# Kernel tuning notes

Hardware: AMD Instinct MI355X
Metric: run time of the kernel (lower is better)

Reference implementation:

```python
import jax, jax.numpy as jnp
import numpy as np

B, H, W = 2, 64, 1024
C1, C2 = 64, 128
MLP = [128, 128]
KH, KW = 5, 5
NS = 3
DIST = 100.0
BN_EPS = 1e-5


def setup_inputs() -> dict:
    key = jax.random.key(0)
    ks = jax.random.split(key, 12)
    inp = {
        "xyz1_proj": jax.random.normal(ks[0], (B, H, W, 3), jnp.float32),
        "xyz2_proj": jax.random.normal(ks[1], (B, H, W, 3), jnp.float32),
        "feat1_proj": jax.random.normal(ks[2], (B, H, W, C1), jnp.float32),
        "feat2_proj": jax.random.normal(ks[3], (B, H, W, C2), jnp.float32),
    }
    cin = C1 + C2
    chans = [cin] + MLP
    for i in range(len(MLP)):
        inp[f"w{i}"] = jax.random.normal(ks[4 + 2 * i], (chans[i], chans[i + 1]), jnp.float32) * 0.05
        inp[f"b{i}"] = jnp.zeros((chans[i + 1],), jnp.float32)
        inp[f"g{i}"] = jnp.ones((chans[i + 1],), jnp.float32)
        inp[f"be{i}"] = jnp.zeros((chans[i + 1],), jnp.float32)
    return inp


def _grid_knn(xyz1, xyz2):
    """Structured-grid KNN (no_sort_knn): for each query pixel, scan a KHxKW
    window in row-major order and take the first NS in-bounds neighbors whose
    squared distance is below DIST^2. Returns flat neighbor indices (B,N,NS)
    and a validity mask (B,N,NS,1)."""
    b, h, w, _ = xyz1.shape
    n = h * w
    k = KH * KW
    x1 = xyz1.reshape(b, n, 3)
    x2 = xyz2.reshape(b, n, 3)
    oh = jnp.repeat(jnp.arange(KH) - KH // 2, KW)   # (K,)
    ow = jnp.tile(jnp.arange(KW) - KW // 2, KH)     # (K,)
    nh = jnp.arange(h)[:, None, None] + oh[None, None, :]   # (H,1,K)
    nw = jnp.arange(w)[None, :, None] + ow[None, None, :]   # (1,W,K)
    inb = ((nh >= 0) & (nh < h)) & ((nw >= 0) & (nw < w))    # (H,W,K)
    flat = jnp.clip(nh, 0, h - 1) * w + jnp.clip(nw, 0, w - 1)
    flat = jnp.broadcast_to(flat, (h, w, k)).reshape(n, k)
    inb = jnp.broadcast_to(inb, (h, w, k)).reshape(n, k)
    # window gather: (B,N,K,3)
    neigh = jnp.take(x2, flat.reshape(-1), axis=1).reshape(b, n, k, 3)
    sq = jnp.sum(jnp.square(neigh - x1[:, :, None, :]), -1)  # (B,N,K)
    valid = inb[None] & (sq < DIST * DIST)
    v = valid.astype(jnp.int32)
    rank = jnp.cumsum(v, -1) - v  # rank among valid, scan order
    sel, fnd = [], []
    for j in range(NS):
        hit = valid & (rank == j)
        sel.append(jnp.argmax(hit, -1))
        fnd.append(jnp.any(hit, -1))
    sel = jnp.stack(sel, -1)          # (B,N,NS) window slot
    found = jnp.stack(fnd, -1)        # (B,N,NS)
    flat_b = jnp.broadcast_to(flat[None], (b, n, k))
    sel_flat = jnp.take_along_axis(flat_b, sel, axis=-1)
    sel_flat = jnp.where(found, sel_flat, 0)  # zeros like the init buffers
    mask = found.astype(x1.dtype)[..., None]  # (B,N,NS,1)
    return sel_flat, mask


def _gather(feat_flat, sel_flat):
    # feat_flat: (B,N,C), sel_flat: (B,N,NS) -> (B,N,NS,C)
    b, n, c = feat_flat.shape
    idx = sel_flat.reshape(b, n * NS, 1)
    g = jnp.take_along_axis(feat_flat, jnp.broadcast_to(idx, (b, n * NS, c)), axis=1)
    return g.reshape(b, n, NS, c)


def reference(xyz1_proj, xyz2_proj, feat1_proj, feat2_proj,
              w0, b0, g0, be0, w1, b1, g1, be1):
    b, h, w, _ = xyz1_proj.shape
    n = h * w
    xyz1 = xyz1_proj.reshape(b, n, 3)
    xyz2 = xyz2_proj.reshape(b, n, 3)
    feat2 = feat2_proj.reshape(b, n, -1)

    sel_flat, mask = _grid_knn(xyz1_proj, xyz2_proj)
    mask = jax.lax.stop_gradient(mask)

    grouped_xyz = _gather(xyz2, sel_flat) * mask          # (B,N,NS,3)
    grouped_feat = _gather(feat2, sel_flat) * mask        # (B,N,NS,C2)

    dist = jnp.sum(jnp.square(grouped_xyz - xyz1[:, :, None, :]), -1)  # (B,N,NS)
    dist = jnp.where(dist < 1e-10, jnp.full_like(dist, 1e-10), dist)
    norm = jnp.sum(1.0 / dist, axis=2, keepdims=True)     # (B,N,1)
    weight = (1.0 / dist) / norm                          # (B,N,NS)
    interp = jnp.sum(grouped_feat * weight[..., None], axis=2)  # (B,N,C2)

    x = jnp.concatenate([feat1_proj.reshape(b, n, -1), interp], -1)  # (B,N,C1+C2)

    # 1x1 conv MLP with training-mode BatchNorm + ReLU
    for (wi, bi, gi, bei) in ((w0, b0, g0, be0), (w1, b1, g1, be1)):
        x = x @ wi + bi
        mu = jnp.mean(x, axis=(0, 1))
        var = jnp.var(x, axis=(0, 1))
        x = (x - mu) * jax.lax.rsqrt(var + BN_EPS) * gi + bei
        x = jax.nn.relu(x)
    return x  # (B, H*W, MLP[-1])
```

## Files before the change

kernel.cpp:

```cpp
#include <hip/hip_runtime.h>

#define H_    64
#define W_    1024
#define NPT   65536
#define NTOT  131072
#define C1_   64
#define C2_   128
#define CIN_  192
#define CM_   128
#define NS_   3
#define DIST2_ 10000.0f
#define BN_EPS_ 1e-5f
#define NSLOT 32

typedef __attribute__((ext_vector_type(8))) short short8;
typedef __attribute__((ext_vector_type(4))) float floatx4;

static __device__ __forceinline__ unsigned short f2bf(float f) {
    unsigned int u = __float_as_uint(f);
    u += 0x7fffu + ((u >> 16) & 1u);
    return (unsigned short)(u >> 16);
}
static __device__ __forceinline__ float bflo(unsigned u) { return __uint_as_float(u << 16); }
static __device__ __forceinline__ float bfhi(unsigned u) { return __uint_as_float(u & 0xffff0000u); }
static __device__ __forceinline__ unsigned packbf(float a, float b) {
    return (unsigned)f2bf(a) | ((unsigned)f2bf(b) << 16);
}

__global__ __launch_bounds__(256) void prepw_kernel(
    const float* __restrict__ w0, const float* __restrict__ w1,
    unsigned short* __restrict__ w0F, unsigned short* __restrict__ w1F)
{
    int tid = blockIdx.x * 256 + threadIdx.x;
    if (tid < 3072) {
        int c = tid, lane = c & 63, nt = (c >> 6) & 7, kk = c >> 9;
        int n = nt * 16 + (lane & 15);
        int kb = kk * 32 + (lane >> 4) * 8;
        #pragma unroll
        for (int j = 0; j < 8; j++)
            w0F[(size_t)c * 8 + j] = f2bf(w0[(size_t)(kb + j) * CM_ + n]);
    } else if (tid < 5120) {
        int c = tid - 3072, lane = c & 63, nt = (c >> 6) & 7, kk = c >> 9;
        int n = nt * 16 + (lane & 15);
        int kb = kk * 32 + (lane >> 4) * 8;
        #pragma unroll
        for (int j = 0; j < 8; j++)
            w1F[(size_t)c * 8 + j] = f2bf(w1[(size_t)(kb + j) * CM_ + n]);
    }
}

__global__ __launch_bounds__(256, 3) void fused1_kernel(
    const float* __restrict__ xyz1, const float* __restrict__ xyz2,
    const float* __restrict__ feat1, const float* __restrict__ feat2,
    const unsigned short* __restrict__ w0F, const float* __restrict__ b0,
    uint2* __restrict__ y0w, float* __restrict__ slots0)
{
    __shared__ unsigned short xstage[128][CM_ + 8];
    __shared__ int   selL[128][NS_];
    __shared__ float wgtL[128][NS_];
    __shared__ float wsum[4][CM_], wsq[4][CM_];

    const int t = threadIdx.x;
    const int blk = blockIdx.x;
    const int pbase = blk * 128;
    const int bidx = blk >> 9;
    const int wv = t >> 6, lane = t & 63;
    const int m = lane & 15, q = lane >> 4;
    const int row0 = pbase + wv * 16 + m;
    const int row1 = row0 + 64;

    if (t < 128) {
        int pt = pbase + t;
        int n = pt & (NPT - 1);
        int h = n >> 10, w = n & (W_ - 1);
        const float* p1 = xyz1 + (size_t)pt * 3;
        float x1 = p1[0], y1 = p1[1], z1 = p1[2];
        const float* x2b = xyz2 + (size_t)bidx * NPT * 3;
        int s0 = 0, s1 = 0, s2 = 0;
        float d0 = 0.f, d1 = 0.f, d2 = 0.f;
        int cnt = 0;
        for (int dh = -2; dh <= 2; dh++) {
            int nh = h + dh;
            bool okh = (nh >= 0) && (nh < H_);
            for (int dw = -2; dw <= 2; dw++) {
                int nw = w + dw;
                if (!(okh && nw >= 0 && nw < W_)) continue;
                int nidx = nh * W_ + nw;
                const float* p2 = x2b + (size_t)nidx * 3;
                float dx = p2[0] - x1, dy = p2[1] - y1, dz = p2[2] - z1;
                float sq = dx * dx + dy * dy + dz * dz;
                if (sq < DIST2_ && cnt < NS_) {
                    if (cnt == 0)      { s0 = nidx; d0 = sq; }
                    else if (cnt == 1) { s1 = nidx; d1 = sq; }
                    else               { s2 = nidx; d2 = sq; }
                    cnt++;
                }
            }
        }
        float self2 = x1 * x1 + y1 * y1 + z1 * z1;
        float dd0 = (cnt > 0) ? d0 : self2;
        float dd1 = (cnt > 1) ? d1 : self2;
        float dd2 = (cnt > 2) ? d2 : self2;
        dd0 = fmaxf(dd0, 1e-10f); dd1 = fmaxf(dd1, 1e-10f); dd2 = fmaxf(dd2, 1e-10f);
        float i0 = 1.0f / dd0, i1 = 1.0f / dd1, i2 = 1.0f / dd2;
        float norm = i0 + i1 + i2;
        selL[t][0] = (cnt > 0) ? s0 : 0;
        selL[t][1] = (cnt > 1) ? s1 : 0;
        selL[t][2] = (cnt > 2) ? s2 : 0;
        wgtL[t][0] = (cnt > 0) ? i0 / norm : 0.f;
        wgtL[t][1] = (cnt > 1) ? i1 / norm : 0.f;
        wgtL[t][2] = (cnt > 2) ? i2 / norm : 0.f;
    }

    short8 af0[2], af1[2];
    #pragma unroll
    for (int kk = 0; kk < 2; kk++) {
        const float* s0p = feat1 + (size_t)row0 * C1_ + kk * 32 + q * 8;
        const float* s1p = feat1 + (size_t)row1 * C1_ + kk * 32 + q * 8;
        float4 fa = *(const float4*)(s0p), fb = *(const float4*)(s0p + 4);
        float4 ga = *(const float4*)(s1p), gb = *(const float4*)(s1p + 4);
        short8 a, b;
        a[0] = f2bf(fa.x); a[1] = f2bf(fa.y); a[2] = f2bf(fa.z); a[3] = f2bf(fa.w);
        a[4] = f2bf(fb.x); a[5] = f2bf(fb.y); a[6] = f2bf(fb.z); a[7] = f2bf(fb.w);
        b[0] = f2bf(ga.x); b[1] = f2bf(ga.y); b[2] = f2bf(ga.z); b[3] = f2bf(ga.w);
        b[4] = f2bf(gb.x); b[5] = f2bf(gb.y); b[6] = f2bf(gb.z); b[7] = f2bf(gb.w);
        af0[kk] = a; af1[kk] = b;
    }
    __syncthreads();

    const float* f2b = feat2 + (size_t)bidx * NPT * C2_;
    #pragma unroll
    for (int i = 0; i < 16; i++) {
        int idx = t + i * 256;
        int p = idx >> 5, c4 = (idx & 31) << 2;
        float ax = 0.f, ay = 0.f, az = 0.f, aw = 0.f;
        #pragma unroll
        for (int j = 0; j < NS_; j++) {
            float wj = wgtL[p][j];
            const float4 f = *(const float4*)(f2b + (size_t)selL[p][j] * C2_ + c4);
            ax += wj * f.x; ay += wj * f.y; az += wj * f.z; aw += wj * f.w;
        }
        ushort4 u;
        u.x = f2bf(ax); u.y = f2bf(ay); u.z = f2bf(az); u.w = f2bf(aw);
        *(ushort4*)&xstage[p][c4] = u;
    }
    __syncthreads();

    floatx4 acc0[8], acc1[8];
    #pragma unroll
    for (int nt = 0; nt < 8; nt++) {
        acc0[nt] = (floatx4){0.f, 0.f, 0.f, 0.f};
        acc1[nt] = (floatx4){0.f, 0.f, 0.f, 0.f};
    }

    const int lr0 = wv * 16 + m, lr1 = lr0 + 64;
    #pragma unroll
    for (int kk = 0; kk < 6; kk++) {
        short8 bw[8];
        #pragma unroll
        for (int nt = 0; nt < 8; nt++)
            bw[nt] = *(const short8*)(w0F + ((size_t)(kk * 8 + nt) * 64 + lane) * 8);
        short8 a0, a1;
        if (kk < 2) { a0 = af0[kk]; a1 = af1[kk]; }
        else {
            a0 = *(const short8*)&xstage[lr0][(kk - 2) * 32 + q * 8];
            a1 = *(const short8*)&xstage[lr1][(kk - 2) * 32 + q * 8];
        }
        #pragma unroll
        for (int nt = 0; nt < 8; nt++) {
            acc0[nt] = __builtin_amdgcn_mfma_f32_16x16x32_bf16(a0, bw[nt], acc0[nt], 0, 0, 0);
            acc1[nt] = __builtin_amdgcn_mfma_f32_16x16x32_bf16(a1, bw[nt], acc1[nt], 0, 0, 0);
        }
    }

    #pragma unroll
    for (int nt = 0; nt < 8; nt++) {
        int n = nt * 16 + m;
        float bv = b0[n];
        unsigned u0 = packbf(acc0[nt][0] + bv, acc0[nt][1] + bv);
        unsigned u1 = packbf(acc0[nt][2] + bv, acc0[nt][3] + bv);
        unsigned u2 = packbf(acc1[nt][0] + bv, acc1[nt][1] + bv);
        unsigned u3 = packbf(acc1[nt][2] + bv, acc1[nt][3] + bv);
        int g0i = blk * 2;
        y0w[((size_t)(g0i * 4 + wv) * 8 + nt) * 64 + lane]       = make_uint2(u0, u1);
        y0w[((size_t)((g0i + 1) * 4 + wv) * 8 + nt) * 64 + lane] = make_uint2(u2, u3);
        float v0 = bflo(u0), v1 = bfhi(u0), v2 = bflo(u1), v3 = bfhi(u1);
        float v4 = bflo(u2), v5 = bfhi(u2), v6 = bflo(u3), v7 = bfhi(u3);
        float s  = v0 + v1 + v2 + v3 + v4 + v5 + v6 + v7;
        float q2 = v0*v0 + v1*v1 + v2*v2 + v3*v3 + v4*v4 + v5*v5 + v6*v6 + v7*v7;
        s += __shfl_xor(s, 16, 64); q2 += __shfl_xor(q2, 16, 64);
        s += __shfl_xor(s, 32, 64); q2 += __shfl_xor(q2, 32, 64);
        if (q == 0) { wsum[wv][n] = s; wsq[wv][n] = q2; }
    }
    __syncthreads();

    float* slot = slots0 + (size_t)(blk & (NSLOT - 1)) * 256;
    if (t < CM_)
        atomicAdd(&slot[t], wsum[0][t] + wsum[1][t] + wsum[2][t] + wsum[3][t]);
    else
        atomicAdd(&slot[t], wsq[0][t - CM_] + wsq[1][t - CM_] + wsq[2][t - CM_] + wsq[3][t - CM_]);
}

__global__ __launch_bounds__(256, 3) void fused2_kernel(
    const uint2* __restrict__ y0w, const float* __restrict__ slots0,
    const float* __restrict__ g0, const float* __restrict__ be0,
    const unsigned short* __restrict__ w1F, const float* __restrict__ b1,
    uint2* __restrict__ y1w, float* __restrict__ slots1)
{
    __shared__ unsigned short x1s[128][CM_ + 8];
    __shared__ float scl[CM_], shf[CM_];
    __shared__ float wsum[4][CM_], wsq[4][CM_];

    const int t = threadIdx.x;
    const int blk = blockIdx.x;
    const int wv = t >> 6, lane = t & 63;
    const int m = lane & 15, q = lane >> 4;
    const int g0i = blk * 2;

    if (t < CM_) {
        float s = 0.f, q2 = 0.f;
        #pragma unroll
        for (int sl = 0; sl < NSLOT; sl++) {
            s  += slots0[sl * 256 + t];
            q2 += slots0[sl * 256 + CM_ + t];
        }
        const float invn = 1.0f / (float)NTOT;
        float mu = s * invn, var = q2 * invn - mu * mu;
        float sc = g0[t] * rsqrtf(var + BN_EPS_);
        scl[t] = sc; shf[t] = be0[t] - mu * sc;
    }
    __syncthreads();

    #pragma unroll
    for (int nt = 0; nt < 8; nt++) {
        int n = nt * 16 + m;
        float sc = scl[n], sh = shf[n];
        uint2 ua = y0w[((size_t)(g0i * 4 + wv) * 8 + nt) * 64 + lane];
        uint2 ub = y0w[((size_t)((g0i + 1) * 4 + wv) * 8 + nt) * 64 + lane];
        int rb = wv * 16 + q * 4;
        x1s[rb + 0][n] = f2bf(fmaxf(bflo(ua.x) * sc + sh, 0.f));
        x1s[rb + 1][n] = f2bf(fmaxf(bfhi(ua.x) * sc + sh, 0.f));
        x1s[rb + 2][n] = f2bf(fmaxf(bflo(ua.y) * sc + sh, 0.f));
        x1s[rb + 3][n] = f2bf(fmaxf(bfhi(ua.y) * sc + sh, 0.f));
        x1s[64 + rb + 0][n] = f2bf(fmaxf(bflo(ub.x) * sc + sh, 0.f));
        x1s[64 + rb + 1][n] = f2bf(fmaxf(bfhi(ub.x) * sc + sh, 0.f));
        x1s[64 + rb + 2][n] = f2bf(fmaxf(bflo(ub.y) * sc + sh, 0.f));
        x1s[64 + rb + 3][n] = f2bf(fmaxf(bfhi(ub.y) * sc + sh, 0.f));
    }
    __syncthreads();

    const int lr0 = wv * 16 + m, lr1 = lr0 + 64;
    floatx4 acc0[8], acc1[8];
    #pragma unroll
    for (int nt = 0; nt < 8; nt++) {
        acc0[nt] = (floatx4){0.f, 0.f, 0.f, 0.f};
        acc1[nt] = (floatx4){0.f, 0.f, 0.f, 0.f};
    }

    #pragma unroll
    for (int kk = 0; kk < 4; kk++) {
        short8 bw[8];
        #pragma unroll
        for (int nt = 0; nt < 8; nt++)
            bw[nt] = *(const short8*)(w1F + ((size_t)(kk * 8 + nt) * 64 + lane) * 8);
        short8 a0 = *(const short8*)&x1s[lr0][kk * 32 + q * 8];
        short8 a1 = *(const short8*)&x1s[lr1][kk * 32 + q * 8];
        #pragma unroll
        for (int nt = 0; nt < 8; nt++) {
            acc0[nt] = __builtin_amdgcn_mfma_f32_16x16x32_bf16(a0, bw[nt], acc0[nt], 0, 0, 0);
            acc1[nt] = __builtin_amdgcn_mfma_f32_16x16x32_bf16(a1, bw[nt], acc1[nt], 0, 0, 0);
        }
    }

    #pragma unroll
    for (int nt = 0; nt < 8; nt++) {
        int n = nt * 16 + m;
        float bv = b1[n];
        unsigned u0 = packbf(acc0[nt][0] + bv, acc0[nt][1] + bv);
        unsigned u1 = packbf(acc0[nt][2] + bv, acc0[nt][3] + bv);
        unsigned u2 = packbf(acc1[nt][0] + bv, acc1[nt][1] + bv);
        unsigned u3 = packbf(acc1[nt][2] + bv, acc1[nt][3] + bv);
        y1w[((size_t)(g0i * 4 + wv) * 8 + nt) * 64 + lane]       = make_uint2(u0, u1);
        y1w[((size_t)((g0i + 1) * 4 + wv) * 8 + nt) * 64 + lane] = make_uint2(u2, u3);
        float v0 = bflo(u0), v1 = bfhi(u0), v2 = bflo(u1), v3 = bfhi(u1);
        float v4 = bflo(u2), v5 = bfhi(u2), v6 = bflo(u3), v7 = bfhi(u3);
        float s  = v0 + v1 + v2 + v3 + v4 + v5 + v6 + v7;
        float q2 = v0*v0 + v1*v1 + v2*v2 + v3*v3 + v4*v4 + v5*v5 + v6*v6 + v7*v7;
        s += __shfl_xor(s, 16, 64); q2 += __shfl_xor(q2, 16, 64);
        s += __shfl_xor(s, 32, 64); q2 += __shfl_xor(q2, 32, 64);
        if (q == 0) { wsum[wv][n] = s; wsq[wv][n] = q2; }
    }
    __syncthreads();

    float* slot = slots1 + (size_t)(blk & (NSLOT - 1)) * 256;
    if (t < CM_)
        atomicAdd(&slot[t], wsum[0][t] + wsum[1][t] + wsum[2][t] + wsum[3][t]);
    else
        atomicAdd(&slot[t], wsq[0][t - CM_] + wsq[1][t - CM_] + wsq[2][t - CM_] + wsq[3][t - CM_]);
}

__global__ __launch_bounds__(256) void bn_out_kernel(
    const uint2* __restrict__ y1w, const float* __restrict__ slots1,
    const float* __restrict__ g1, const float* __restrict__ be1,
    float* __restrict__ out)
{
    __shared__ float xo[64][CM_ + 12];
    __shared__ float scl[CM_], shf[CM_];
    const int t = threadIdx.x;
    const int blk = blockIdx.x;
    const int wv = t >> 6, lane = t & 63;
    const int m = lane & 15, q = lane >> 4;

    if (t < CM_) {
        float s = 0.f, q2 = 0.f;
        #pragma unroll
        for (int sl = 0; sl < NSLOT; sl++) {
            s  += slots1[sl * 256 + t];
            q2 += slots1[sl * 256 + CM_ + t];
        }
        const float invn = 1.0f / (float)NTOT;
        float mu = s * invn, var = q2 * invn - mu * mu;
        float sc = g1[t] * rsqrtf(var + BN_EPS_);
        scl[t] = sc; shf[t] = be1[t] - mu * sc;
    }
    __syncthreads();

    #pragma unroll
    for (int tile = 0; tile < 2; tile++) {
        const int g = blk * 2 + tile;
        #pragma unroll
        for (int nt = 0; nt < 8; nt++) {
            int n = nt * 16 + m;
            float sc = scl[n], sh = shf[n];
            uint2 u = y1w[((size_t)(g * 4 + wv) * 8 + nt) * 64 + lane];
            int rb = wv * 16 + q * 4;
            xo[rb + 0][n] = fmaxf(bflo(u.x) * sc + sh, 0.f);
            xo[rb + 1][n] = fmaxf(bfhi(u.x) * sc + sh, 0.f);
            xo[rb + 2][n] = fmaxf(bflo(u.y) * sc + sh, 0.f);
            xo[rb + 3][n] = fmaxf(bfhi(u.y) * sc + sh, 0.f);
        }
        __syncthreads();
        const int pbase = g * 64;
        #pragma unroll
        for (int i = 0; i < 8; i++) {
            int idx = t + i * 256;
            int p = idx >> 5, c4 = (idx & 31) << 2;
            float4 v = *(const float4*)&xo[p][c4];
            *(float4*)(out + (size_t)(pbase + p) * CM_ + c4) = v;
        }
        __syncthreads();
    }
}

extern "C" void kernel_launch(void* const* d_in, const int* in_sizes, int n_in,
                              void* d_out, int out_size, void* d_ws, size_t ws_size,
                              hipStream_t stream)
{
    const float* xyz1  = (const float*)d_in[0];
    const float* xyz2  = (const float*)d_in[1];
    const float* feat1 = (const float*)d_in[2];
    const float* feat2 = (const float*)d_in[3];
    const float* w0    = (const float*)d_in[4];
    const float* b0    = (const float*)d_in[5];
    const float* g0    = (const float*)d_in[6];
    const float* be0   = (const float*)d_in[7];
    const float* w1    = (const float*)d_in[8];
    const float* b1    = (const float*)d_in[9];
    const float* g1    = (const float*)d_in[10];
    const float* be1   = (const float*)d_in[11];
    float* out = (float*)d_out;

    char* ws = (char*)d_ws;
    float* slots0       = (float*)(ws);
    float* slots1       = (float*)(ws + (size_t)NSLOT * 256 * 4);
    char*  p            = ws + 2 * (size_t)NSLOT * 256 * 4;
    unsigned short* w0F = (unsigned short*)p;  p += (size_t)CIN_ * CM_ * 2;
    unsigned short* w1F = (unsigned short*)p;  p += (size_t)CM_ * CM_ * 2;
    uint2* y0w          = (uint2*)p;           p += (size_t)NTOT * CM_ * 2;
    uint2* y1w          = (uint2*)p;

    hipMemsetAsync(ws, 0, 2 * (size_t)NSLOT * 256 * 4, stream);

    prepw_kernel<<<20, 256, 0, stream>>>(w0, w1, w0F, w1F);
    fused1_kernel<<<NTOT / 128, 256, 0, stream>>>(xyz1, xyz2, feat1, feat2,
                                                  w0F, b0, y0w, slots0);
    fused2_kernel<<<NTOT / 128, 256, 0, stream>>>(y0w, slots0, g0, be0,
                                                  w1F, b1, y1w, slots1);
    bn_out_kernel<<<NTOT / 128, 256, 0, stream>>>(y1w, slots1, g1, be1, out);
}
```

Measured before the change: 227.0 us.

## Fuse three stages into one persistent kernel with grid-wide barriers for BatchNorm stats

Replaces the three kernels (gather+GEMM0, BN0+GEMM1, BN1+output) with one kernel of 512 blocks. Each block handles 256 points, keeps the layer outputs in registers, and uses atomic-counter spin barriers to wait for the global BatchNorm statistics. This removes the bf16 intermediate round-trips through global memory and two launches. The cost is lower occupancy (launch bounds 3 to 2), higher register pressure, and a reliance on all 512 blocks being co-resident or the barrier deadlocks.

```diff
diff --git a/kernel.cpp b/kernel.cpp
--- a/kernel.cpp
+++ b/kernel.cpp
@@ -12,6 +12,7 @@
 #define DIST2_ 10000.0f
 #define BN_EPS_ 1e-5f
 #define NSLOT 32
+#define GRID_ 512
 
 typedef __attribute__((ext_vector_type(8))) short short8;
 typedef __attribute__((ext_vector_type(4))) float floatx4;
@@ -49,28 +50,35 @@
     }
 }
 
-__global__ __launch_bounds__(256, 3) void fused1_kernel(
+__global__ __launch_bounds__(256, 2) void mega_kernel(
     const float* __restrict__ xyz1, const float* __restrict__ xyz2,
     const float* __restrict__ feat1, const float* __restrict__ feat2,
     const unsigned short* __restrict__ w0F, const float* __restrict__ b0,
-    uint2* __restrict__ y0w, float* __restrict__ slots0)
+    const float* __restrict__ g0, const float* __restrict__ be0,
+    const unsigned short* __restrict__ w1F, const float* __restrict__ b1,
+    const float* __restrict__ g1, const float* __restrict__ be1,
+    float* __restrict__ out, int* __restrict__ cnt,
+    float* __restrict__ slots0, float* __restrict__ slots1)
 {
-    __shared__ unsigned short xstage[128][CM_ + 8];
-    __shared__ int   selL[128][NS_];
-    __shared__ float wgtL[128][NS_];
+    __shared__ __align__(16) char buf[35840];
+    __shared__ int   selL[256][NS_];
+    __shared__ float wgtL[256][NS_];
     __shared__ float wsum[4][CM_], wsq[4][CM_];
+    __shared__ float scl[CM_], shf[CM_];
+
+    unsigned short (*xst)[CM_ + 8] = (unsigned short (*)[CM_ + 8])buf;
+    float (*xo)[CM_ + 12] = (float (*)[CM_ + 12])buf;
 
     const int t = threadIdx.x;
     const int blk = blockIdx.x;
-    const int pbase = blk * 128;
-    const int bidx = blk >> 9;
+    const int pblock = blk * 256;
+    const int bidx = blk >> 8;
     const int wv = t >> 6, lane = t & 63;
     const int m = lane & 15, q = lane >> 4;
-    const int row0 = pbase + wv * 16 + m;
-    const int row1 = row0 + 64;
-
-    if (t < 128) {
-        int pt = pbase + t;
+    const float* f2b = feat2 + (size_t)bidx * NPT * C2_;
+
+    {
+        int pt = pblock + t;
         int n = pt & (NPT - 1);
         int h = n >> 10, w = n & (W_ - 1);
         const float* p1 = xyz1 + (size_t)pt * 3;
@@ -78,7 +86,7 @@
         const float* x2b = xyz2 + (size_t)bidx * NPT * 3;
         int s0 = 0, s1 = 0, s2 = 0;
         float d0 = 0.f, d1 = 0.f, d2 = 0.f;
-        int cnt = 0;
+        int cnt_ = 0;
         for (int dh = -2; dh <= 2; dh++) {
             int nh = h + dh;
             bool okh = (nh >= 0) && (nh < H_);
@@ -89,140 +97,147 @@
                 const float* p2 = x2b + (size_t)nidx * 3;
                 float dx = p2[0] - x1, dy = p2[1] - y1, dz = p2[2] - z1;
                 float sq = dx * dx + dy * dy + dz * dz;
-                if (sq < DIST2_ && cnt < NS_) {
-                    if (cnt == 0)      { s0 = nidx; d0 = sq; }
-                    else if (cnt == 1) { s1 = nidx; d1 = sq; }
-                    else               { s2 = nidx; d2 = sq; }
-                    cnt++;
+                if (sq < DIST2_ && cnt_ < NS_) {
+                    if (cnt_ == 0)      { s0 = nidx; d0 = sq; }
+                    else if (cnt_ == 1) { s1 = nidx; d1 = sq; }
+                    else                { s2 = nidx; d2 = sq; }
+                    cnt_++;
                 }
             }
         }
         float self2 = x1 * x1 + y1 * y1 + z1 * z1;
-        float dd0 = (cnt > 0) ? d0 : self2;
-        float dd1 = (cnt > 1) ? d1 : self2;
-        float dd2 = (cnt > 2) ? d2 : self2;
+        float dd0 = (cnt_ > 0) ? d0 : self2;
+        float dd1 = (cnt_ > 1) ? d1 : self2;
+        float dd2 = (cnt_ > 2) ? d2 : self2;
         dd0 = fmaxf(dd0, 1e-10f); dd1 = fmaxf(dd1, 1e-10f); dd2 = fmaxf(dd2, 1e-10f);
         float i0 = 1.0f / dd0, i1 = 1.0f / dd1, i2 = 1.0f / dd2;
         float norm = i0 + i1 + i2;
-        selL[t][0] = (cnt > 0) ? s0 : 0;
-        selL[t][1] = (cnt > 1) ? s1 : 0;
-        selL[t][2] = (cnt > 2) ? s2 : 0;
-        wgtL[t][0] = (cnt > 0) ? i0 / norm : 0.f;
-        wgtL[t][1] = (cnt > 1) ? i1 / norm : 0.f;
-        wgtL[t][2] = (cnt > 2) ? i2 / norm : 0.f;
-    }
-
-    short8 af0[2], af1[2];
-    #pragma unroll
-    for (int kk = 0; kk < 2; kk++) {
-        const float* s0p = feat1 + (size_t)row0 * C1_ + kk * 32 + q * 8;
-        const float* s1p = feat1 + (size_t)row1 * C1_ + kk * 32 + q * 8;
-        float4 fa = *(const float4*)(s0p), fb = *(const float4*)(s0p + 4);
-        float4 ga = *(const float4*)(s1p), gb = *(const float4*)(s1p + 4);
-        short8 a, b;
-        a[0] = f2bf(fa.x); a[1] = f2bf(fa.y); a[2] = f2bf(fa.z); a[3] = f2bf(fa.w);
-        a[4] = f2bf(fb.x); a[5] = f2bf(fb.y); a[6] = f2bf(fb.z); a[7] = f2bf(fb.w);
-        b[0] = f2bf(ga.x); b[1] = f2bf(ga.y); b[2] = f2bf(ga.z); b[3] = f2bf(ga.w);
-        b[4] = f2bf(gb.x); b[5] = f2bf(gb.y); b[6] = f2bf(gb.z); b[7] = f2bf(gb.w);
-        af0[kk] = a; af1[kk] = b;
-    }
-    __syncthreads();
-
-    const float* f2b = feat2 + (size_t)bidx * NPT * C2_;
-    #pragma unroll
-    for (int i = 0; i < 16; i++) {
-        int idx = t + i * 256;
-        int p = idx >> 5, c4 = (idx & 31) << 2;
-        float ax = 0.f, ay = 0.f, az = 0.f, aw = 0.f;
-        #pragma unroll
-        for (int j = 0; j < NS_; j++) {
-            float wj = wgtL[p][j];
-            const float4 f = *(const float4*)(f2b + (size_t)selL[p][j] * C2_ + c4);
-            ax += wj * f.x; ay += wj * f.y; az += wj * f.z; aw += wj * f.w;
-        }
-        ushort4 u;
-        u.x = f2bf(ax); u.y = f2bf(ay); u.z = f2bf(az); u.w = f2bf(aw);
-        *(ushort4*)&xstage[p][c4] = u;
-    }
-    __syncthreads();
-
-    floatx4 acc0[8], acc1[8];
+        selL[t][0] = (cnt_ > 0) ? s0 : 0;
+        selL[t][1] = (cnt_ > 1) ? s1 : 0;
+        selL[t][2] = (cnt_ > 2) ? s2 : 0;
+        wgtL[t][0] = (cnt_ > 0) ? i0 / norm : 0.f;
+        wgtL[t][1] = (cnt_ > 1) ? i1 / norm : 0.f;
+        wgtL[t][2] = (cnt_ > 2) ? i2 / norm : 0.f;
+    }
+    __syncthreads();
+
+    uint2 yr[2][2][8];
+    float csum[8], csq[8];
+    #pragma unroll
+    for (int nt = 0; nt < 8; nt++) { csum[nt] = 0.f; csq[nt] = 0.f; }
+
+    #pragma unroll
+    for (int g = 0; g < 2; g++) {
+        const int pbase = pblock + g * 128;
+        const int row0 = pbase + wv * 16 + m, row1 = row0 + 64;
+
+        short8 af0[2], af1[2];
+        #pragma unroll
+        for (int kk = 0; kk < 2; kk++) {
+            const float* s0p = feat1 + (size_t)row0 * C1_ + kk * 32 + q * 8;
+            const float* s1p = feat1 + (size_t)row1 * C1_ + kk * 32 + q * 8;
+            float4 fa = *(const float4*)(s0p), fb = *(const float4*)(s0p + 4);
+            float4 ga = *(const float4*)(s1p), gb = *(const float4*)(s1p + 4);
+            short8 a, b;
+            a[0] = f2bf(fa.x); a[1] = f2bf(fa.y); a[2] = f2bf(fa.z); a[3] = f2bf(fa.w);
+            a[4] = f2bf(fb.x); a[5] = f2bf(fb.y); a[6] = f2bf(fb.z); a[7] = f2bf(fb.w);
+            b[0] = f2bf(ga.x); b[1] = f2bf(ga.y); b[2] = f2bf(ga.z); b[3] = f2bf(ga.w);
+            b[4] = f2bf(gb.x); b[5] = f2bf(gb.y); b[6] = f2bf(gb.z); b[7] = f2bf(gb.w);
+            af0[kk] = a; af1[kk] = b;
+        }
+
+        #pragma unroll
+        for (int i = 0; i < 16; i++) {
+            int idx = t + i * 256;
+            int p = idx >> 5, c4 = (idx & 31) << 2;
+            int lp = g * 128 + p;
+            float ax = 0.f, ay = 0.f, az = 0.f, aw = 0.f;
+            #pragma unroll
+            for (int j = 0; j < NS_; j++) {
+                float wj = wgtL[lp][j];
+                const float4 f = *(const float4*)(f2b + (size_t)selL[lp][j] * C2_ + c4);
+                ax += wj * f.x; ay += wj * f.y; az += wj * f.z; aw += wj * f.w;
+            }
+            ushort4 u;
+            u.x = f2bf(ax); u.y = f2bf(ay); u.z = f2bf(az); u.w = f2bf(aw);
+            *(ushort4*)&xst[p][c4] = u;
+        }
+        __syncthreads();
+
+        floatx4 acc0[8], acc1[8];
+        #pragma unroll
+        for (int nt = 0; nt < 8; nt++) {
+            acc0[nt] = (floatx4){0.f, 0.f, 0.f, 0.f};
+            acc1[nt] = (floatx4){0.f, 0.f, 0.f, 0.f};
+        }
+        const int lr0 = wv * 16 + m, lr1 = lr0 + 64;
+        #pragma unroll
+        for (int kk = 0; kk < 6; kk++) {
+            short8 bw[8];
+            #pragma unroll
+            for (int nt = 0; nt < 8; nt++)
+                bw[nt] = *(const short8*)(w0F + ((size_t)(kk * 8 + nt) * 64 + lane) * 8);
+            short8 a0, a1;
+            if (kk < 2) { a0 = af0[kk]; a1 = af1[kk]; }
+            else {
+                a0 = *(const short8*)&xst[lr0][(kk - 2) * 32 + q * 8];
+                a1 = *(const short8*)&xst[lr1][(kk - 2) * 32 + q * 8];
+            }
+            #pragma unroll
+            for (int nt = 0; nt < 8; nt++) {
+                acc0[nt] = __builtin_amdgcn_mfma_f32_16x16x32_bf16(a0, bw[nt], acc0[nt], 0, 0, 0);
+                acc1[nt] = __builtin_amdgcn_mfma_f32_16x16x32_bf16(a1, bw[nt], acc1[nt], 0, 0, 0);
+            }
+        }
+        #pragma unroll
+        for (int nt = 0; nt < 8; nt++) {
+            int n = nt * 16 + m;
+            float bv = b0[n];
+            unsigned u0 = packbf(acc0[nt][0] + bv, acc0[nt][1] + bv);
+            unsigned u1 = packbf(acc0[nt][2] + bv, acc0[nt][3] + bv);
+            unsigned u2 = packbf(acc1[nt][0] + bv, acc1[nt][1] + bv);
+            unsigned u3 = packbf(acc1[nt][2] + bv, acc1[nt][3] + bv);
+            yr[g][0][nt] = make_uint2(u0, u1);
+            yr[g][1][nt] = make_uint2(u2, u3);
+            float v0 = bflo(u0), v1 = bfhi(u0), v2 = bflo(u1), v3 = bfhi(u1);
+            float v4 = bflo(u2), v5 = bfhi(u2), v6 = bflo(u3), v7 = bfhi(u3);
+            csum[nt] += v0 + v1 + v2 + v3 + v4 + v5 + v6 + v7;
+            csq[nt]  += v0*v0 + v1*v1 + v2*v2 + v3*v3 + v4*v4 + v5*v5 + v6*v6 + v7*v7;
+        }
+        __syncthreads();
+    }
+
     #pragma unroll
     for (int nt = 0; nt < 8; nt++) {
-        acc0[nt] = (floatx4){0.f, 0.f, 0.f, 0.f};
-        acc1[nt] = (floatx4){0.f, 0.f, 0.f, 0.f};
-    }
-
-    const int lr0 = wv * 16 + m, lr1 = lr0 + 64;
-    #pragma unroll
-    for (int kk = 0; kk < 6; kk++) {
-        short8 bw[8];
-        #pragma unroll
-        for (int nt = 0; nt < 8; nt++)
-            bw[nt] = *(const short8*)(w0F + ((size_t)(kk * 8 + nt) * 64 + lane) * 8);
-        short8 a0, a1;
-        if (kk < 2) { a0 = af0[kk]; a1 = af1[kk]; }
-        else {
-            a0 = *(const short8*)&xstage[lr0][(kk - 2) * 32 + q * 8];
-            a1 = *(const short8*)&xstage[lr1][(kk - 2) * 32 + q * 8];
-        }
-        #pragma unroll
-        for (int nt = 0; nt < 8; nt++) {
-            acc0[nt] = __builtin_amdgcn_mfma_f32_16x16x32_bf16(a0, bw[nt], acc0[nt], 0, 0, 0);
-            acc1[nt] = __builtin_amdgcn_mfma_f32_16x16x32_bf16(a1, bw[nt], acc1[nt], 0, 0, 0);
-        }
-    }
-
-    #pragma unroll
-    for (int nt = 0; nt < 8; nt++) {
-        int n = nt * 16 + m;
-        float bv = b0[n];
-        unsigned u0 = packbf(acc0[nt][0] + bv, acc0[nt][1] + bv);
-        unsigned u1 = packbf(acc0[nt][2] + bv, acc0[nt][3] + bv);
-        unsigned u2 = packbf(acc1[nt][0] + bv, acc1[nt][1] + bv);
-        unsigned u3 = packbf(acc1[nt][2] + bv, acc1[nt][3] + bv);
-        int g0i = blk * 2;
-        y0w[((size_t)(g0i * 4 + wv) * 8 + nt) * 64 + lane]       = make_uint2(u0, u1);
-        y0w[((size_t)((g0i + 1) * 4 + wv) * 8 + nt) * 64 + lane] = make_uint2(u2, u3);
-        float v0 = bflo(u0), v1 = bfhi(u0), v2 = bflo(u1), v3 = bfhi(u1);
-        float v4 = bflo(u2), v5 = bfhi(u2), v6 = bflo(u3), v7 = bfhi(u3);
-        float s  = v0 + v1 + v2 + v3 + v4 + v5 + v6 + v7;
-        float q2 = v0*v0 + v1*v1 + v2*v2 + v3*v3 + v4*v4 + v5*v5 + v6*v6 + v7*v7;
+        float s = csum[nt], q2 = csq[nt];
         s += __shfl_xor(s, 16, 64); q2 += __shfl_xor(q2, 16, 64);
         s += __shfl_xor(s, 32, 64); q2 += __shfl_xor(q2, 32, 64);
-        if (q == 0) { wsum[wv][n] = s; wsq[wv][n] = q2; }
-    }
-    __syncthreads();
-
-    float* slot = slots0 + (size_t)(blk & (NSLOT - 1)) * 256;
-    if (t < CM_)
-        atomicAdd(&slot[t], wsum[0][t] + wsum[1][t] + wsum[2][t] + wsum[3][t]);
-    else
-        atomicAdd(&slot[t], wsq[0][t - CM_] + wsq[1][t - CM_] + wsq[2][t - CM_] + wsq[3][t - CM_]);
-}
-
-__global__ __launch_bounds__(256, 3) void fused2_kernel(
-    const uint2* __restrict__ y0w, const float* __restrict__ slots0,
-    const float* __restrict__ g0, const float* __restrict__ be0,
-    const unsigned short* __restrict__ w1F, const float* __restrict__ b1,
-    uint2* __restrict__ y1w, float* __restrict__ slots1)
-{
-    __shared__ unsigned short x1s[128][CM_ + 8];
-    __shared__ float scl[CM_], shf[CM_];
-    __shared__ float wsum[4][CM_], wsq[4][CM_];
-
-    const int t = threadIdx.x;
-    const int blk = blockIdx.x;
-    const int wv = t >> 6, lane = t & 63;
-    const int m = lane & 15, q = lane >> 4;
-    const int g0i = blk * 2;
+        if (q == 0) { wsum[wv][nt * 16 + m] = s; wsq[wv][nt * 16 + m] = q2; }
+    }
+    __syncthreads();
+    {
+        float* slot = slots0 + (size_t)(blk & (NSLOT - 1)) * 256;
+        if (t < CM_)
+            atomicAdd(&slot[t], wsum[0][t] + wsum[1][t] + wsum[2][t] + wsum[3][t]);
+        else
+            atomicAdd(&slot[t], wsq[0][t-CM_] + wsq[1][t-CM_] + wsq[2][t-CM_] + wsq[3][t-CM_]);
+    }
+
+    __syncthreads();
+    if (t == 0) {
+        __threadfence();
+        atomicAdd(&cnt[0], 1);
+        while (__hip_atomic_load(&cnt[0], __ATOMIC_ACQUIRE, __HIP_MEMORY_SCOPE_AGENT) < GRID_)
+            __builtin_amdgcn_s_sleep(8);
+    }
+    __syncthreads();
 
     if (t < CM_) {
         float s = 0.f, q2 = 0.f;
         #pragma unroll
         for (int sl = 0; sl < NSLOT; sl++) {
-            s  += slots0[sl * 256 + t];
-            q2 += slots0[sl * 256 + CM_ + t];
+            s  += __hip_atomic_load(&slots0[sl * 256 + t],       __ATOMIC_RELAXED, __HIP_MEMORY_SCOPE_AGENT);
+            q2 += __hip_atomic_load(&slots0[sl * 256 + CM_ + t], __ATOMIC_RELAXED, __HIP_MEMORY_SCOPE_AGENT);
         }
         const float invn = 1.0f / (float)NTOT;
         float mu = s * invn, var = q2 * invn - mu * mu;
@@ -232,91 +247,99 @@
     __syncthreads();
 
     #pragma unroll
+    for (int nt = 0; nt < 8; nt++) { csum[nt] = 0.f; csq[nt] = 0.f; }
+    float sclv[8], shfv[8];
+    #pragma unroll
+    for (int nt = 0; nt < 8; nt++) { sclv[nt] = scl[nt * 16 + m]; shfv[nt] = shf[nt * 16 + m]; }
+
+    #pragma unroll
+    for (int g = 0; g < 2; g++) {
+        #pragma unroll
+        for (int nt = 0; nt < 8; nt++) {
+            int n = nt * 16 + m;
+            uint2 ua = yr[g][0][nt], ub = yr[g][1][nt];
+            int rb = wv * 16 + q * 4;
+            xst[rb + 0][n] = f2bf(fmaxf(bflo(ua.x) * sclv[nt] + shfv[nt], 0.f));
+            xst[rb + 1][n] = f2bf(fmaxf(bfhi(ua.x) * sclv[nt] + shfv[nt], 0.f));
+            xst[rb + 2][n] = f2bf(fmaxf(bflo(ua.y) * sclv[nt] + shfv[nt], 0.f));
+            xst[rb + 3][n] = f2bf(fmaxf(bfhi(ua.y) * sclv[nt] + shfv[nt], 0.f));
+            xst[64 + rb + 0][n] = f2bf(fmaxf(bflo(ub.x) * sclv[nt] + shfv[nt], 0.f));
+            xst[64 + rb + 1][n] = f2bf(fmaxf(bfhi(ub.x) * sclv[nt] + shfv[nt], 0.f));
+            xst[64 + rb + 2][n] = f2bf(fmaxf(bflo(ub.y) * sclv[nt] + shfv[nt], 0.f));
+            xst[64 + rb + 3][n] = f2bf(fmaxf(bfhi(ub.y) * sclv[nt] + shfv[nt], 0.f));
+        }
+        __syncthreads();
+
+        const int lr0 = wv * 16 + m, lr1 = lr0 + 64;
+        floatx4 acc0[8], acc1[8];
+        #pragma unroll
+        for (int nt = 0; nt < 8; nt++) {
+            acc0[nt] = (floatx4){0.f, 0.f, 0.f, 0.f};
+            acc1[nt] = (floatx4){0.f, 0.f, 0.f, 0.f};
+        }
+        #pragma unroll
+        for (int kk = 0; kk < 4; kk++) {
+            short8 bw[8];
+            #pragma unroll
+            for (int nt = 0; nt < 8; nt++)
+                bw[nt] = *(const short8*)(w1F + ((size_t)(kk * 8 + nt) * 64 + lane) * 8);
+            short8 a0 = *(const short8*)&xst[lr0][kk * 32 + q * 8];
+            short8 a1 = *(const short8*)&xst[lr1][kk * 32 + q * 8];
+            #pragma unroll
+            for (int nt = 0; nt < 8; nt++) {
+                acc0[nt] = __builtin_amdgcn_mfma_f32_16x16x32_bf16(a0, bw[nt], acc0[nt], 0, 0, 0);
+                acc1[nt] = __builtin_amdgcn_mfma_f32_16x16x32_bf16(a1, bw[nt], acc1[nt], 0, 0, 0);
+            }
+        }
+        #pragma unroll
+        for (int nt = 0; nt < 8; nt++) {
+            int n = nt * 16 + m;
+            float bv = b1[n];
+            unsigned u0 = packbf(acc0[nt][0] + bv, acc0[nt][1] + bv);
+            unsigned u1 = packbf(acc0[nt][2] + bv, acc0[nt][3] + bv);
+            unsigned u2 = packbf(acc1[nt][0] + bv, acc1[nt][1] + bv);
+            unsigned u3 = packbf(acc1[nt][2] + bv, acc1[nt][3] + bv);
+            yr[g][0][nt] = make_uint2(u0, u1);
+            yr[g][1][nt] = make_uint2(u2, u3);
+            float v0 = bflo(u0), v1 = bfhi(u0), v2 = bflo(u1), v3 = bfhi(u1);
+            float v4 = bflo(u2), v5 = bfhi(u2), v6 = bflo(u3), v7 = bfhi(u3);
+            csum[nt] += v0 + v1 + v2 + v3 + v4 + v5 + v6 + v7;
+            csq[nt]  += v0*v0 + v1*v1 + v2*v2 + v3*v3 + v4*v4 + v5*v5 + v6*v6 + v7*v7;
+        }
+        __syncthreads();
+    }
+
+    #pragma unroll
     for (int nt = 0; nt < 8; nt++) {
-        int n = nt * 16 + m;
-        float sc = scl[n], sh = shf[n];
-        uint2 ua = y0w[((size_t)(g0i * 4 + wv) * 8 + nt) * 64 + lane];
-        uint2 ub = y0w[((size_t)((g0i + 1) * 4 + wv) * 8 + nt) * 64 + lane];
-        int rb = wv * 16 + q * 4;
-        x1s[rb + 0][n] = f2bf(fmaxf(bflo(ua.x) * sc + sh, 0.f));
-        x1s[rb + 1][n] = f2bf(fmaxf(bfhi(ua.x) * sc + sh, 0.f));
-        x1s[rb + 2][n] = f2bf(fmaxf(bflo(ua.y) * sc + sh, 0.f));
-        x1s[rb + 3][n] = f2bf(fmaxf(bfhi(ua.y) * sc + sh, 0.f));
-        x1s[64 + rb + 0][n] = f2bf(fmaxf(bflo(ub.x) * sc + sh, 0.f));
-        x1s[64 + rb + 1][n] = f2bf(fmaxf(bfhi(ub.x) * sc + sh, 0.f));
-        x1s[64 + rb + 2][n] = f2bf(fmaxf(bflo(ub.y) * sc + sh, 0.f));
-        x1s[64 + rb + 3][n] = f2bf(fmaxf(bfhi(ub.y) * sc + sh, 0.f));
-    }
-    __syncthreads();
-
-    const int lr0 = wv * 16 + m, lr1 = lr0 + 64;
-    floatx4 acc0[8], acc1[8];
-    #pragma unroll
-    for (int nt = 0; nt < 8; nt++) {
-        acc0[nt] = (floatx4){0.f, 0.f, 0.f, 0.f};
-        acc1[nt] = (floatx4){0.f, 0.f, 0.f, 0.f};
-    }
-
-    #pragma unroll
-    for (int kk = 0; kk < 4; kk++) {
-        short8 bw[8];
-        #pragma unroll
-        for (int nt = 0; nt < 8; nt++)
-            bw[nt] = *(const short8*)(w1F + ((size_t)(kk * 8 + nt) * 64 + lane) * 8);
-        short8 a0 = *(const short8*)&x1s[lr0][kk * 32 + q * 8];
-        short8 a1 = *(const short8*)&x1s[lr1][kk * 32 + q * 8];
-        #pragma unroll
-        for (int nt = 0; nt < 8; nt++) {
-            acc0[nt] = __builtin_amdgcn_mfma_f32_16x16x32_bf16(a0, bw[nt], acc0[nt], 0, 0, 0);
-            acc1[nt] = __builtin_amdgcn_mfma_f32_16x16x32_bf16(a1, bw[nt], acc1[nt], 0, 0, 0);
-        }
-    }
-
-    #pragma unroll
-    for (int nt = 0; nt < 8; nt++) {
-        int n = nt * 16 + m;
-        float bv = b1[n];
-        unsigned u0 = packbf(acc0[nt][0] + bv, acc0[nt][1] + bv);
-        unsigned u1 = packbf(acc0[nt][2] + bv, acc0[nt][3] + bv);
-        unsigned u2 = packbf(acc1[nt][0] + bv, acc1[nt][1] + bv);
-        unsigned u3 = packbf(acc1[nt][2] + bv, acc1[nt][3] + bv);
-        y1w[((size_t)(g0i * 4 + wv) * 8 + nt) * 64 + lane]       = make_uint2(u0, u1);
-        y1w[((size_t)((g0i + 1) * 4 + wv) * 8 + nt) * 64 + lane] = make_uint2(u2, u3);
-        float v0 = bflo(u0), v1 = bfhi(u0), v2 = bflo(u1), v3 = bfhi(u1);
-        float v4 = bflo(u2), v5 = bfhi(u2), v6 = bflo(u3), v7 = bfhi(u3);
-        float s  = v0 + v1 + v2 + v3 + v4 + v5 + v6 + v7;
-        float q2 = v0*v0 + v1*v1 + v2*v2 + v3*v3 + v4*v4 + v5*v5 + v6*v6 + v7*v7;
+        float s = csum[nt], q2 = csq[nt];
         s += __shfl_xor(s, 16, 64); q2 += __shfl_xor(q2, 16, 64);
         s += __shfl_xor(s, 32, 64); q2 += __shfl_xor(q2, 32, 64);
-        if (q == 0) { wsum[wv][n] = s; wsq[wv][n] = q2; }
-    }
-    __syncthreads();
-
-    float* slot = slots1 + (size_t)(blk & (NSLOT - 1)) * 256;
-    if (t < CM_)
-        atomicAdd(&slot[t], wsum[0][t] + wsum[1][t] + wsum[2][t] + wsum[3][t]);
-    else
-        atomicAdd(&slot[t], wsq[0][t - CM_] + wsq[1][t - CM_] + wsq[2][t - CM_] + wsq[3][t - CM_]);
-}
-
-__global__ __launch_bounds__(256) void bn_out_kernel(
-    const uint2* __restrict__ y1w, const float* __restrict__ slots1,
-    const float* __restrict__ g1, const float* __restrict__ be1,
-    float* __restrict__ out)
-{
-    __shared__ float xo[64][CM_ + 12];
-    __shared__ float scl[CM_], shf[CM_];
-    const int t = threadIdx.x;
-    const int blk = blockIdx.x;
-    const int wv = t >> 6, lane = t & 63;
-    const int m = lane & 15, q = lane >> 4;
+        if (q == 0) { wsum[wv][nt * 16 + m] = s; wsq[wv][nt * 16 + m] = q2; }
+    }
+    __syncthreads();
+    {
+        float* slot = slots1 + (size_t)(blk & (NSLOT - 1)) * 256;
+        if (t < CM_)
+            atomicAdd(&slot[t], wsum[0][t] + wsum[1][t] + wsum[2][t] + wsum[3][t]);
+        else
+            atomicAdd(&slot[t], wsq[0][t-CM_] + wsq[1][t-CM_] + wsq[2][t-CM_] + wsq[3][t-CM_]);
+    }
+
+    __syncthreads();
+    if (t == 0) {
+        __threadfence();
+        atomicAdd(&cnt[1], 1);
+        while (__hip_atomic_load(&cnt[1], __ATOMIC_ACQUIRE, __HIP_MEMORY_SCOPE_AGENT) < GRID_)
+            __builtin_amdgcn_s_sleep(8);
+    }
+    __syncthreads();
 
     if (t < CM_) {
         float s = 0.f, q2 = 0.f;
         #pragma unroll
         for (int sl = 0; sl < NSLOT; sl++) {
-            s  += slots1[sl * 256 + t];
-            q2 += slots1[sl * 256 + CM_ + t];
+            s  += __hip_atomic_load(&slots1[sl * 256 + t],       __ATOMIC_RELAXED, __HIP_MEMORY_SCOPE_AGENT);
+            q2 += __hip_atomic_load(&slots1[sl * 256 + CM_ + t], __ATOMIC_RELAXED, __HIP_MEMORY_SCOPE_AGENT);
         }
         const float invn = 1.0f / (float)NTOT;
         float mu = s * invn, var = q2 * invn - mu * mu;
@@ -326,29 +349,31 @@
     __syncthreads();
 
     #pragma unroll
-    for (int tile = 0; tile < 2; tile++) {
-        const int g = blk * 2 + tile;
-        #pragma unroll
-        for (int nt = 0; nt < 8; nt++) {
-            int n = nt * 16 + m;
-            float sc = scl[n], sh = shf[n];
-            uint2 u = y1w[((size_t)(g * 4 + wv) * 8 + nt) * 64 + lane];
-            int rb = wv * 16 + q * 4;
-            xo[rb + 0][n] = fmaxf(bflo(u.x) * sc + sh, 0.f);
-            xo[rb + 1][n] = fmaxf(bfhi(u.x) * sc + sh, 0.f);
-            xo[rb + 2][n] = fmaxf(bflo(u.y) * sc + sh, 0.f);
-            xo[rb + 3][n] = fmaxf(bfhi(u.y) * sc + sh, 0.f);
-        }
-        __syncthreads();
-        const int pbase = g * 64;
-        #pragma unroll
-        for (int i = 0; i < 8; i++) {
-            int idx = t + i * 256;
-            int p = idx >> 5, c4 = (idx & 31) << 2;
-            float4 v = *(const float4*)&xo[p][c4];
-            *(float4*)(out + (size_t)(pbase + p) * CM_ + c4) = v;
-        }
-        __syncthreads();
+    for (int g = 0; g < 2; g++) {
+        #pragma unroll
+        for (int tile = 0; tile < 2; tile++) {
+            #pragma unroll
+            for (int nt = 0; nt < 8; nt++) {
+                int n = nt * 16 + m;
+                float sc = scl[n], sh = shf[n];
+                uint2 u = yr[g][tile][nt];
+                int rb = wv * 16 + q * 4;
+                xo[rb + 0][n] = fmaxf(bflo(u.x) * sc + sh, 0.f);
+                xo[rb + 1][n] = fmaxf(bfhi(u.x) * sc + sh, 0.f);
+                xo[rb + 2][n] = fmaxf(bflo(u.y) * sc + sh, 0.f);
+                xo[rb + 3][n] = fmaxf(bfhi(u.y) * sc + sh, 0.f);
+            }
+            __syncthreads();
+            const int pbase = pblock + g * 128 + tile * 64;
+            #pragma unroll
+            for (int i = 0; i < 8; i++) {
+                int idx = t + i * 256;
+                int p = idx >> 5, c4 = (idx & 31) << 2;
+                float4 v = *(const float4*)&xo[p][c4];
+                *(float4*)(out + (size_t)(pbase + p) * CM_ + c4) = v;
+            }
+            __syncthreads();
+        }
     }
 }
 
@@ -371,20 +396,18 @@
     float* out = (float*)d_out;
 
     char* ws = (char*)d_ws;
-    float* slots0       = (float*)(ws);
-    float* slots1       = (float*)(ws + (size_t)NSLOT * 256 * 4);
-    char*  p            = ws + 2 * (size_t)NSLOT * 256 * 4;
+    int*   cnt          = (int*)ws;
+    float* slots0       = (float*)(ws + 1024);
+    float* slots1       = (float*)(ws + 1024 + (size_t)NSLOT * 256 * 4);
+    char*  p            = ws + 1024 + 2 * (size_t)NSLOT * 256 * 4;
     unsigned short* w0F = (unsigned short*)p;  p += (size_t)CIN_ * CM_ * 2;
-    unsigned short* w1F = (unsigned short*)p;  p += (size_t)CM_ * CM_ * 2;
-    uint2* y0w          = (uint2*)p;           p += (size_t)NTOT * CM_ * 2;
-    uint2* y1w          = (uint2*)p;
-
-    hipMemsetAsync(ws, 0, 2 * (size_t)NSLOT * 256 * 4, stream);
+    unsigned short* w1F = (unsigned short*)p;
+
+    hipMemsetAsync(ws, 0, 1024 + 2 * (size_t)NSLOT * 256 * 4, stream);
 
     prepw_kernel<<<20, 256, 0, stream>>>(w0, w1, w0F, w1F);
-    fused1_kernel<<<NTOT / 128, 256, 0, stream>>>(xyz1, xyz2, feat1, feat2,
-                                                  w0F, b0, y0w, slots0);
-    fused2_kernel<<<NTOT / 128, 256, 0, stream>>>(y0w, slots0, g0, be0,
-                                                  w1F, b1, y1w, slots1);
-    bn_out_kernel<<<NTOT / 128, 256, 0, stream>>>(y1w, slots1, g1, be1, out);
+    mega_kernel<<<GRID_, 256, 0, stream>>>(xyz1, xyz2, feat1, feat2,
+                                           w0F, b0, g0, be0,
+                                           w1F, b1, g1, be1,
+                                           out, cnt, slots0, slots1);
 }
```

New measurement: 266.9 us. +17.6%, slower.
